# Performance work log

Hardware: AMD Instinct MI355X
Metric: run time of the kernel (lower is better)

## Reference

```python
import jax, jax.numpy as jnp
import numpy as np

B, S, H = 1, 2048, 2048
HD, NQ, NKV = 128, 16, 4
FFH = 8192
EPS = 1e-5
ROPE_BASE = 10000.0
SOFTMAX_CAP = 50.0
CLIP_L, CLIP_R = 0.0, 1.0


def setup_inputs() -> dict:
    key = jax.random.key(0)
    ks = jax.random.split(key, 10)
    std = 0.02
    return {
        "x": jax.random.normal(ks[0], (B, S, H), dtype=jnp.float32),
        "attn_norm_w": jax.random.uniform(ks[1], (H,), minval=-1.0, maxval=1.0, dtype=jnp.float32),
        "mlp_norm_w": jax.random.uniform(ks[2], (H,), minval=-1.0, maxval=1.0, dtype=jnp.float32),
        "wq": jax.random.normal(ks[3], (H, NQ * HD), dtype=jnp.float32) * std,
        "wk": jax.random.normal(ks[4], (H, NKV * HD), dtype=jnp.float32) * std,
        "wv": jax.random.normal(ks[5], (H, NKV * HD), dtype=jnp.float32) * std,
        "wo": jax.random.normal(ks[6], (NQ * HD, H), dtype=jnp.float32) * std,
        "w_gate": jax.random.normal(ks[7], (H, FFH), dtype=jnp.float32) * std,
        "w_up": jax.random.normal(ks[8], (H, FFH), dtype=jnp.float32) * std,
        "w_down": jax.random.normal(ks[9], (FFH, H), dtype=jnp.float32) * std,
    }


def _rms_norm(x, w):
    # GroupRMSNorm with group_size=None -> whole hidden dim
    var = jnp.mean(jnp.square(x), axis=-1, keepdims=True)
    return x * jax.lax.rsqrt(var + EPS) * w


def _rope_cos_sin(seq_len, dim):
    inv_freq = 1.0 / (ROPE_BASE ** (jnp.arange(0, dim, 2, dtype=jnp.float32) / dim))
    t = jnp.arange(seq_len, dtype=jnp.float32)
    freqs = jnp.outer(t, inv_freq)                      # [S, dim/2]
    emb = jnp.concatenate([freqs, freqs], axis=-1)      # [S, dim]
    return jnp.cos(emb), jnp.sin(emb)


def _apply_rope(x, cos, sin):
    # x: [B, S, h, d]; rotate-half (LLaMA-style)
    d = x.shape[-1]
    x1, x2 = x[..., : d // 2], x[..., d // 2 :]
    rot = jnp.concatenate([-x2, x1], axis=-1)
    return x * cos[None, :, None, :] + rot * sin[None, :, None, :]


def _qk_norm(x):
    # per-head RMS norm over head_dim (qk_norm_group_size == head_dim), unit weight
    var = jnp.mean(jnp.square(x), axis=-1, keepdims=True)
    return x * jax.lax.rsqrt(var + EPS)


def reference(x, attn_norm_w, mlp_norm_w, wq, wk, wv, wo, w_gate, w_up, w_down):
    # ---- attention sub-layer ----
    h = _rms_norm(x, attn_norm_w)                                     # [B,S,H]
    q = (h @ wq).reshape(B, S, NQ, HD)
    k = (h @ wk).reshape(B, S, NKV, HD)
    v = (h @ wv).reshape(B, S, NKV, HD)

    cos, sin = _rope_cos_sin(S, HD)
    q = _apply_rope(q, cos, sin)
    k = _apply_rope(k, cos, sin)

    q = _qk_norm(q)
    k = _qk_norm(k)

    # GQA: expand kv heads to match q heads
    rep = NQ // NKV
    k = jnp.repeat(k, rep, axis=2)                                    # [B,S,NQ,HD]
    v = jnp.repeat(v, rep, axis=2)

    scale = 1.0 / jnp.sqrt(jnp.float32(HD))
    scores = jnp.einsum("bshd,bthd->bhst", q, k) * scale              # [B,NQ,S,S]
    # softmax cap: cap * tanh(s / cap)
    scores = SOFTMAX_CAP * jnp.tanh(scores / SOFTMAX_CAP)
    causal = jnp.tril(jnp.ones((S, S), dtype=bool))
    scores = jnp.where(causal[None, None], scores, -jnp.inf)
    p = jax.nn.softmax(scores, axis=-1)
    # clip range (l, r): clamp(p * (r - l) + l, 0, 1)
    p = jnp.clip(p * (CLIP_R - CLIP_L) + CLIP_L, 0.0, 1.0)
    o = jnp.einsum("bhst,bthd->bshd", p, v).reshape(B, S, NQ * HD)
    x = x + o @ wo

    # ---- MLP sub-layer (gated SiLU) ----
    h2 = _rms_norm(x, mlp_norm_w)
    mlp_out = (jax.nn.silu(h2 @ w_gate) * (h2 @ w_up)) @ w_down
    return x + mlp_out
```

## Files before the change

kernel.cpp:

```cpp
#include <hip/hip_runtime.h>

typedef __bf16 bf16;
typedef __bf16 bf16x4 __attribute__((ext_vector_type(4)));
typedef __bf16 bf16x8 __attribute__((ext_vector_type(8)));
typedef float f32x4 __attribute__((ext_vector_type(4)));

#define GLP16(gp, lp) __builtin_amdgcn_global_load_lds( \
    (const __attribute__((address_space(1))) void*)(gp), \
    (__attribute__((address_space(3))) void*)(lp), 16, 0, 0)

__device__ __forceinline__ f32x4 mfma16(bf16x8 a, bf16x8 b, f32x4 c) {
    return __builtin_amdgcn_mfma_f32_16x16x32_bf16(a, b, c, 0, 0, 0);
}

__global__ __launch_bounds__(256) void k_rmsnorm(const float* __restrict__ x,
        const float* __restrict__ w, bf16* __restrict__ out) {
    const int H = 2048;
    size_t row = blockIdx.x;
    const float* xr = x + row * H;
    int base = threadIdx.x * 8;
    float4 a = *(const float4*)(xr + base);
    float4 b = *(const float4*)(xr + base + 4);
    float ss = a.x*a.x + a.y*a.y + a.z*a.z + a.w*a.w
             + b.x*b.x + b.y*b.y + b.z*b.z + b.w*b.w;
#pragma unroll
    for (int m = 32; m > 0; m >>= 1) ss += __shfl_xor(ss, m);
    __shared__ float red[4];
    if ((threadIdx.x & 63) == 0) red[threadIdx.x >> 6] = ss;
    __syncthreads();
    float tot = red[0] + red[1] + red[2] + red[3];
    float rs = rsqrtf(tot * (1.0f / H) + 1e-5f);
    float4 wa = *(const float4*)(w + base);
    float4 wb = *(const float4*)(w + base + 4);
    bf16x8 ov;
    ov[0] = (bf16)(a.x * rs * wa.x); ov[1] = (bf16)(a.y * rs * wa.y);
    ov[2] = (bf16)(a.z * rs * wa.z); ov[3] = (bf16)(a.w * rs * wa.w);
    ov[4] = (bf16)(b.x * rs * wb.x); ov[5] = (bf16)(b.y * rs * wb.y);
    ov[6] = (bf16)(b.z * rs * wb.z); ov[7] = (bf16)(b.w * rs * wb.w);
    *(bf16x8*)(out + row * H + base) = ov;
}

__global__ __launch_bounds__(256) void k_convT(const float* __restrict__ W,
        bf16* __restrict__ Wt, int K, int N, int rmul, int roff) {
    __shared__ float t[32][33];
    int k0 = blockIdx.x * 32, n0 = blockIdx.y * 32;
    int tx = threadIdx.x, ty = threadIdx.y;
#pragma unroll
    for (int i = 0; i < 4; i++)
        t[ty + i * 8][tx] = W[(size_t)(k0 + ty + i * 8) * N + n0 + tx];
    __syncthreads();
#pragma unroll
    for (int i = 0; i < 4; i++)
        Wt[((size_t)(n0 + ty + i * 8) * rmul + roff) * K + k0 + tx] =
            (bf16)t[tx][ty + i * 8];
}

__global__ __launch_bounds__(256) void k_transpose(const bf16* __restrict__ in,
        bf16* __restrict__ out, int R, int C) {
    __shared__ bf16 t[32][33];
    int r0 = blockIdx.x * 32, c0 = blockIdx.y * 32;
    int tx = threadIdx.x & 31, ty = threadIdx.x >> 5;
#pragma unroll
    for (int i = 0; i < 4; i++)
        t[ty + i * 8][tx] = in[(size_t)(r0 + ty + i * 8) * C + c0 + tx];
    __syncthreads();
#pragma unroll
    for (int i = 0; i < 4; i++)
        out[(size_t)(c0 + ty + i * 8) * R + r0 + tx] = t[tx][ty + i * 8];
}

template<int EPI>
__global__ __launch_bounds__(512, 2) void k_gemm5(const bf16* __restrict__ A,
        const bf16* __restrict__ Bt, void* __restrict__ outp,
        const void* __restrict__ aux, int M, int N, int K, int ksplit) {
    extern __shared__ char lds[];
    const int tid = threadIdx.x, wave = tid >> 6, lane = tid & 63;
    const int lr = lane & 15, kg = lane >> 4;
    const int wm = wave >> 2, wn = wave & 3;
    const int bn = blockIdx.x, bm = blockIdx.y, split = blockIdx.z;
    const int row0 = bm * 256, col0 = bn * 256;
    const int kbeg = split * ksplit;
    const int NT = ksplit >> 6;
    const size_t K2 = (size_t)K * 2;
    const int xorm = (lr & 7) << 4;

    char* const A0p = lds;
    char* const A1p = lds + 32768;
    char* const B0p = lds + 65536;
    char* const B1p = lds + 98304;

    size_t soff[2];
#pragma unroll
    for (int s = 0; s < 2; s++) {
        int d = s * 8192 + tid * 16;
        int rh = d >> 7, c = d & 127;
        soff[s] = (size_t)rh * K2 + (c ^ ((rh & 7) << 4));
    }
    const char* Ab = (const char*)A + ((size_t)row0 * K + kbeg) * 2;
    const char* Bb = (const char*)Bt + ((size_t)col0 * K + kbeg) * 2;

    auto stA = [&](int t, int mh) {
        const char* src = Ab + (size_t)(mh * 128) * K2 + (size_t)t * 128;
        char* dst = lds + (t & 1) * 32768 + mh * 16384 + wave * 1024;
        GLP16(src + soff[0], dst);
        GLP16(src + soff[1], dst + 8192);
    };
    auto stB = [&](int t, int nh) {
        const char* src = Bb + (size_t)(nh * 128) * K2 + (size_t)t * 128;
        char* dst = lds + 65536 + (t & 1) * 32768 + nh * 16384 + wave * 1024;
        GLP16(src + soff[0], dst);
        GLP16(src + soff[1], dst + 8192);
    };

    f32x4 acc[8][4];
#pragma unroll
    for (int m = 0; m < 8; m++)
#pragma unroll
        for (int n = 0; n < 4; n++) acc[m][n] = (f32x4){0, 0, 0, 0};

    bf16x8 a[8], c0[4], c1[4];
    auto rdA = [&](const char* base, int mh) {
#pragma unroll
        for (int mi = 0; mi < 4; mi++)
#pragma unroll
            for (int kk = 0; kk < 2; kk++) {
                int rh = wm * 64 + mi * 16 + lr;
                int c = (kk * 64 + kg * 16) ^ xorm;
                a[mi * 2 + kk] = *(const bf16x8*)(base + mh * 16384 + rh * 128 + c);
            }
    };
    auto rdB = [&](const char* base, int nh, bf16x8 (&b)[4]) {
#pragma unroll
        for (int nj = 0; nj < 2; nj++)
#pragma unroll
            for (int kk = 0; kk < 2; kk++) {
                int rh = wn * 32 + nj * 16 + lr;
                int c = (kk * 64 + kg * 16) ^ xorm;
                b[nj * 2 + kk] = *(const bf16x8*)(base + nh * 16384 + rh * 128 + c);
            }
    };
    auto mm = [&](int mh, int nh, bf16x8 (&b)[4]) {
#pragma unroll
        for (int mi = 0; mi < 4; mi++)
#pragma unroll
            for (int nj = 0; nj < 2; nj++)
#pragma unroll
                for (int kk = 0; kk < 2; kk++)
                    acc[mh * 4 + mi][nh * 2 + nj] =
                        mfma16(a[mi * 2 + kk], b[nj * 2 + kk],
                               acc[mh * 4 + mi][nh * 2 + nj]);
    };

#define PBAR do { asm volatile("" ::: "memory"); \
                  __builtin_amdgcn_s_barrier(); \
                  asm volatile("" ::: "memory"); } while (0)

    stA(0, 0); stB(0, 0); stB(0, 1); stA(0, 1);
    stA(1, 0); stB(1, 0); stB(1, 1);
    asm volatile("s_waitcnt vmcnt(6)" ::: "memory");
    PBAR;

    const int NIT = NT >> 1;
    for (int it = 0; it < NIT; ++it) {
        const int t = it * 2;
        const bool more = (t + 2 < NT);
        rdA(A0p, 0); rdB(B0p, 0, c0);
        stA(t + 1, 1);
        __builtin_amdgcn_s_setprio(1); mm(0, 0, c0); __builtin_amdgcn_s_setprio(0);
        PBAR;
        rdB(B0p, 1, c1);
        if (more) stA(t + 2, 0);
        __builtin_amdgcn_s_setprio(1); mm(0, 1, c1); __builtin_amdgcn_s_setprio(0);
        PBAR;
        rdA(A0p, 1);
        if (more) stB(t + 2, 0);
        __builtin_amdgcn_s_setprio(1); mm(1, 1, c1); __builtin_amdgcn_s_setprio(0);
        PBAR;
        if (more) stB(t + 2, 1);
        __builtin_amdgcn_s_setprio(1); mm(1, 0, c0); __builtin_amdgcn_s_setprio(0);
        if (more) asm volatile("s_waitcnt vmcnt(6)" ::: "memory");
        else      asm volatile("s_waitcnt vmcnt(0)" ::: "memory");
        PBAR;
        rdA(A1p, 0); rdB(B1p, 0, c0);
        if (more) stA(t + 2, 1);
        __builtin_amdgcn_s_setprio(1); mm(0, 0, c0); __builtin_amdgcn_s_setprio(0);
        PBAR;
        rdB(B1p, 1, c1);
        if (t + 3 < NT) stA(t + 3, 0);
        __builtin_amdgcn_s_setprio(1); mm(0, 1, c1); __builtin_amdgcn_s_setprio(0);
        PBAR;
        rdA(A1p, 1);
        if (t + 3 < NT) stB(t + 3, 0);
        __builtin_amdgcn_s_setprio(1); mm(1, 1, c1); __builtin_amdgcn_s_setprio(0);
        PBAR;
        if (t + 3 < NT) stB(t + 3, 1);
        __builtin_amdgcn_s_setprio(1); mm(1, 0, c0); __builtin_amdgcn_s_setprio(0);
        if (more) asm volatile("s_waitcnt vmcnt(6)" ::: "memory");
        PBAR;
    }
#undef PBAR

#pragma unroll
    for (int mi = 0; mi < 8; mi++)
#pragma unroll
        for (int ni = 0; ni < 4; ni++)
#pragma unroll
            for (int r = 0; r < 4; r++) {
                size_t row = row0 + (mi >> 2) * 128 + wm * 64 + (mi & 3) * 16 + kg * 4 + r;
                size_t col = col0 + (ni >> 1) * 128 + wn * 32 + (ni & 1) * 16 + lr;
                float vv = acc[mi][ni][r];
                if (EPI == 3) {
                    ((float*)outp)[(size_t)split * M * N + row * N + col] = vv;
                } else {
                    float pv = __shfl_xor(vv, 1);
                    float g = (lane & 1) ? pv : vv;
                    float u = (lane & 1) ? vv : pv;
                    float sg = g / (1.0f + __expf(-g));
                    if (!(lane & 1))
                        ((bf16*)outp)[row * (size_t)(N >> 1) + (col >> 1)] =
                            (bf16)(sg * u);
                }
            }
}

__global__ __launch_bounds__(256) void k_reduce(const float* __restrict__ parts,
        const float* __restrict__ resid, float* __restrict__ out,
        int ns, size_t n4) {
    size_t i = (size_t)blockIdx.x * 256 + threadIdx.x;
    if (i >= n4) return;
    float4 acc = ((const float4*)resid)[i];
    for (int s = 0; s < ns; s++) {
        float4 p = ((const float4*)(parts + (size_t)s * n4 * 4))[i];
        acc.x += p.x; acc.y += p.y; acc.z += p.z; acc.w += p.w;
    }
    ((float4*)out)[i] = acc;
}

__global__ __launch_bounds__(256) void k_reduce_rms(const float* __restrict__ parts,
        const float* __restrict__ resid, const float* __restrict__ w,
        float* __restrict__ x2, bf16* __restrict__ hb, int ns) {
    const int H = 2048;
    size_t row = blockIdx.x;
    int base = threadIdx.x * 8;
    const float* rr = resid + row * H + base;
    float4 a = *(const float4*)rr;
    float4 b = *(const float4*)(rr + 4);
    for (int s = 0; s < ns; s++) {
        const float* pp = parts + (size_t)s * H * 2048 + row * H + base;
        float4 pa = *(const float4*)pp;
        float4 pb = *(const float4*)(pp + 4);
        a.x += pa.x; a.y += pa.y; a.z += pa.z; a.w += pa.w;
        b.x += pb.x; b.y += pb.y; b.z += pb.z; b.w += pb.w;
    }
    *(float4*)(x2 + row * H + base) = a;
    *(float4*)(x2 + row * H + base + 4) = b;
    float ss = a.x*a.x + a.y*a.y + a.z*a.z + a.w*a.w
             + b.x*b.x + b.y*b.y + b.z*b.z + b.w*b.w;
#pragma unroll
    for (int m = 32; m > 0; m >>= 1) ss += __shfl_xor(ss, m);
    __shared__ float red[4];
    if ((threadIdx.x & 63) == 0) red[threadIdx.x >> 6] = ss;
    __syncthreads();
    float tot = red[0] + red[1] + red[2] + red[3];
    float rs = rsqrtf(tot * (1.0f / H) + 1e-5f);
    float4 wa = *(const float4*)(w + base);
    float4 wb = *(const float4*)(w + base + 4);
    bf16x8 ov;
    ov[0] = (bf16)(a.x * rs * wa.x); ov[1] = (bf16)(a.y * rs * wa.y);
    ov[2] = (bf16)(a.z * rs * wa.z); ov[3] = (bf16)(a.w * rs * wa.w);
    ov[4] = (bf16)(b.x * rs * wb.x); ov[5] = (bf16)(b.y * rs * wb.y);
    ov[6] = (bf16)(b.z * rs * wb.z); ov[7] = (bf16)(b.w * rs * wb.w);
    *(bf16x8*)(hb + row * H + base) = ov;
}

__global__ __launch_bounds__(256) void k_qkvfin(const float* __restrict__ parts,
        bf16* __restrict__ qb, bf16* __restrict__ kb, bf16* __restrict__ vb) {
    int s = blockIdx.x;
    int col = blockIdx.y * 1024 + threadIdx.x * 4;
    const float* p0 = parts + (size_t)s * 3072 + col;
    const float* p1 = p0 + (size_t)2048 * 3072;
    float4 a = *(const float4*)p0;
    float4 b = *(const float4*)p1;
    a.x += b.x; a.y += b.y; a.z += b.z; a.w += b.w;
    bf16x4 o;
    o[0] = (bf16)a.x; o[1] = (bf16)a.y; o[2] = (bf16)a.z; o[3] = (bf16)a.w;
    if (col < 2048)      *(bf16x4*)(qb + (size_t)s * 2048 + col) = o;
    else if (col < 2560) *(bf16x4*)(kb + (size_t)s * 512 + col - 2048) = o;
    else                 *(bf16x4*)(vb + (size_t)s * 512 + col - 2560) = o;
}

__global__ __launch_bounds__(256) void k_rope(bf16* __restrict__ q,
        bf16* __restrict__ k) {
    int s = blockIdx.x, lane = threadIdx.x & 63;
    int hid = blockIdx.y * 4 + (threadIdx.x >> 6);
    bf16* p;
    if (hid < 16) p = q + (size_t)s * 2048 + hid * 128;
    else          p = k + (size_t)s * 512 + (hid - 16) * 128;
    float x1 = (float)p[lane], x2 = (float)p[lane + 64];
    float f = exp2f((float)lane * -0.2076205059304601f);
    float sn, cs;
    sincosf((float)s * f, &sn, &cs);
    float o1 = x1 * cs - x2 * sn;
    float o2 = x2 * cs + x1 * sn;
    float ss = o1 * o1 + o2 * o2;
#pragma unroll
    for (int m = 32; m > 0; m >>= 1) ss += __shfl_xor(ss, m);
    float rs = rsqrtf(ss * (1.0f / 128.0f) + 1e-5f);
    p[lane] = (bf16)(o1 * rs);
    p[lane + 64] = (bf16)(o2 * rs);
}

__global__ __launch_bounds__(256) void k_attn(const bf16* __restrict__ qg,
        const bf16* __restrict__ kgl, const bf16* __restrict__ vtg,
        bf16* __restrict__ og) {
    extern __shared__ char alds[];
    int pi = blockIdx.x, h = blockIdx.y, kvh = h >> 2;
    int tid = threadIdx.x, wave = tid >> 6, lane = tid & 63;
    int lr = lane & 15, kgrp = lane >> 4;

    int rowQ[4], colQ[4], rowV[4], colV[4];
#pragma unroll
    for (int j = 0; j < 4; j++) {
        int p = j * 4096 + wave * 1024 + lane * 16;
        int ps = p ^ (((p >> 8) & 7) << 4);
        rowQ[j] = ps >> 8; colQ[j] = ps & 255;
        int pv = p ^ (((p >> 7) & 7) << 4);
        rowV[j] = pv >> 7; colV[j] = pv & 127;
    }

    const float C1 = 0.08838834764831845f / 50.0f;
    const float L2E50 = 72.13475204444817f;

#pragma unroll 1
    for (int half = 0; half < 2; ++half) {
        int qt = half ? (31 - pi) : pi;
        int nt = qt + 1;

#pragma unroll
        for (int j = 0; j < 4; j++)
            GLP16((const char*)qg + (size_t)(qt * 64 + rowQ[j]) * 4096 + h * 256 + colQ[j],
                  alds + j * 4096 + wave * 1024);
        for (int t = 0; t < 2 && t < nt; t++) {
#pragma unroll
            for (int j = 0; j < 4; j++)
                GLP16((const char*)kgl + (size_t)(t * 64 + rowQ[j]) * 1024 + kvh * 256 + colQ[j],
                      alds + 16384 + t * 16384 + j * 4096 + wave * 1024);
#pragma unroll
            for (int j = 0; j < 4; j++)
                GLP16((const char*)vtg + (size_t)(kvh * 128 + rowV[j]) * 4096 + t * 128 + colV[j],
                      alds + 49152 + t * 16384 + j * 4096 + wave * 1024);
        }
        if (nt > 1) asm volatile("s_waitcnt vmcnt(8)" ::: "memory");
        else        asm volatile("s_waitcnt vmcnt(0)" ::: "memory");
        __builtin_amdgcn_s_barrier();

        bf16x8 qf[4];
#pragma unroll
        for (int c = 0; c < 4; c++) {
            int b = (wave * 16 + lr) * 256 + c * 64 + kgrp * 16;
            qf[c] = *(const bf16x8*)(alds + (b ^ (((b >> 8) & 7) << 4)));
        }
        f32x4 accO[8];
#pragma unroll
        for (int n = 0; n < 8; n++) accO[n] = (f32x4){0, 0, 0, 0};
        float lsum[4] = {0, 0, 0, 0};
        int qrow = qt * 64 + wave * 16 + kgrp * 4;

        for (int kt = 0; kt < nt; kt++) {
            int buf = kt & 1;
            const char* Kb = alds + 16384 + buf * 16384;
            const char* Vb = alds + 49152 + buf * 16384;
            char* Pb = alds + 81920;
#pragma unroll
            for (int j = 0; j < 4; j++) {
                f32x4 s = {0, 0, 0, 0};
#pragma unroll
                for (int c = 0; c < 4; c++) {
                    int b = (j * 16 + lr) * 256 + c * 64 + kgrp * 16;
                    bf16x8 kf = *(const bf16x8*)(Kb + (b ^ (((b >> 8) & 7) << 4)));
                    s = mfma16(qf[c], kf, s);
                }
                int key = kt * 64 + j * 16 + lr;
#pragma unroll
                for (int r = 0; r < 4; r++) {
                    float y = s[r] * C1;
                    float y2 = y * y;
                    float u = fmaf(y2, 0.13333333f, -0.33333333f);
                    u = fmaf(y2, u, 1.0f);
                    float t5 = y * u;
                    float pe = fmaf(t5, L2E50, -L2E50);
                    float pv = (key <= qrow + r) ? exp2f(pe) : 0.0f;
                    lsum[r] += pv;
                    int wb = (wave * 16 + kgrp * 4 + r) * 128 + (j * 16 + lr) * 2;
                    *(bf16*)(Pb + (wb ^ (((wb >> 7) & 7) << 4))) = (bf16)pv;
                }
            }
            bf16x8 pf[2];
#pragma unroll
            for (int ks2 = 0; ks2 < 2; ks2++) {
                int b = (wave * 16 + lr) * 128 + ks2 * 64 + kgrp * 16;
                pf[ks2] = *(const bf16x8*)(Pb + (b ^ (((b >> 7) & 7) << 4)));
            }
#pragma unroll
            for (int n = 0; n < 8; n++)
#pragma unroll
                for (int ks2 = 0; ks2 < 2; ks2++) {
                    int b = (n * 16 + lr) * 128 + ks2 * 64 + kgrp * 16;
                    bf16x8 vf = *(const bf16x8*)(Vb + (b ^ (((b >> 7) & 7) << 4)));
                    accO[n] = mfma16(pf[ks2], vf, accO[n]);
                }
            __builtin_amdgcn_s_barrier();
            bool more = (kt + 2 < nt);
            if (more) {
                int t = kt + 2;
#pragma unroll
                for (int j = 0; j < 4; j++)
                    GLP16((const char*)kgl + (size_t)(t * 64 + rowQ[j]) * 1024 + kvh * 256 + colQ[j],
                          alds + 16384 + buf * 16384 + j * 4096 + wave * 1024);
#pragma unroll
                for (int j = 0; j < 4; j++)
                    GLP16((const char*)vtg + (size_t)(kvh * 128 + rowV[j]) * 4096 + t * 128 + colV[j],
                          alds + 49152 + buf * 16384 + j * 4096 + wave * 1024);
            }
            if (kt + 1 < nt) {
                if (more) asm volatile("s_waitcnt vmcnt(8)" ::: "memory");
                else      asm volatile("s_waitcnt vmcnt(0)" ::: "memory");
                __builtin_amdgcn_s_barrier();
            }
        }
#pragma unroll
        for (int r = 0; r < 4; r++) {
            float t = lsum[r];
            t += __shfl_xor(t, 1); t += __shfl_xor(t, 2);
            t += __shfl_xor(t, 4); t += __shfl_xor(t, 8);
            lsum[r] = t;
        }
#pragma unroll
        for (int n = 0; n < 8; n++)
#pragma unroll
            for (int r = 0; r < 4; r++) {
                size_t row = qt * 64 + wave * 16 + kgrp * 4 + r;
                og[row * 2048 + h * 128 + n * 16 + lr] = (bf16)(accO[n][r] / lsum[r]);
            }
    }
}

extern "C" void kernel_launch(void* const* d_in, const int* in_sizes, int n_in,
                              void* d_out, int out_size, void* d_ws, size_t ws_size,
                              hipStream_t stream) {
    const float* x      = (const float*)d_in[0];
    const float* attn_w = (const float*)d_in[1];
    const float* mlp_w  = (const float*)d_in[2];
    const float* wq     = (const float*)d_in[3];
    const float* wk     = (const float*)d_in[4];
    const float* wv     = (const float*)d_in[5];
    const float* wo     = (const float*)d_in[6];
    const float* wgate  = (const float*)d_in[7];
    const float* wup    = (const float*)d_in[8];
    const float* wdown  = (const float*)d_in[9];
    float* out = (float*)d_out;
    char* ws = (char*)d_ws;

    const size_t MB = 1024 * 1024;
    bf16* Wqkv = (bf16*)(ws + 0);
    bf16* vt   = (bf16*)(ws + 0);
    float* pO  = (float*)(ws + 0);
    bf16* Wgu  = (bf16*)(ws + 0);
    float* pD  = (float*)(ws + 0);
    bf16* WoT  = (bf16*)(ws + 64 * MB);
    bf16* WdT  = (bf16*)(ws + 64 * MB);
    bf16* hb   = (bf16*)(ws + 96 * MB);
    bf16* qb   = (bf16*)(ws + 104 * MB);
    bf16* kb   = (bf16*)(ws + 112 * MB);
    bf16* vb   = (bf16*)(ws + 114 * MB);
    bf16* ob   = (bf16*)(ws + 116 * MB);
    float* x2  = (float*)(ws + 124 * MB);
    bf16* gb   = (bf16*)(ws + 140 * MB);
    float* pQ  = (float*)(ws + 116 * MB);

    const int LDS5 = 131072;
    hipFuncSetAttribute((const void*)&k_gemm5<3>,
        hipFuncAttributeMaxDynamicSharedMemorySize, LDS5);
    hipFuncSetAttribute((const void*)&k_gemm5<4>,
        hipFuncAttributeMaxDynamicSharedMemorySize, LDS5);
    const int LDSA = 90112;
    hipFuncSetAttribute((const void*)&k_attn,
        hipFuncAttributeMaxDynamicSharedMemorySize, LDSA);

    dim3 cb(32, 8);
    const size_t n4 = (size_t)2048 * 2048 / 4;

    k_rmsnorm<<<2048, 256, 0, stream>>>(x, attn_w, hb);
    k_convT<<<dim3(64, 64), cb, 0, stream>>>(wq, Wqkv, 2048, 2048, 1, 0);
    k_convT<<<dim3(64, 16), cb, 0, stream>>>(wk, Wqkv + 4194304, 2048, 512, 1, 0);
    k_convT<<<dim3(64, 16), cb, 0, stream>>>(wv, Wqkv + 5242880, 2048, 512, 1, 0);
    k_gemm5<3><<<dim3(12, 8, 2), 512, LDS5, stream>>>(hb, Wqkv, pQ, nullptr,
                                                      2048, 3072, 2048, 1024);
    k_qkvfin<<<dim3(2048, 3), 256, 0, stream>>>(pQ, qb, kb, vb);
    k_transpose<<<dim3(64, 16), 256, 0, stream>>>(vb, vt, 2048, 512);
    k_rope<<<dim3(2048, 5), 256, 0, stream>>>(qb, kb);
    k_attn<<<dim3(16, 16), 256, LDSA, stream>>>(qb, kb, vt, ob);
    k_convT<<<dim3(64, 64), cb, 0, stream>>>(wo, WoT, 2048, 2048, 1, 0);
    k_gemm5<3><<<dim3(8, 8, 4), 512, LDS5, stream>>>(ob, WoT, pO, nullptr,
                                                     2048, 2048, 2048, 512);
    k_reduce_rms<<<2048, 256, 0, stream>>>(pO, x, mlp_w, x2, hb, 4);
    k_convT<<<dim3(64, 256), cb, 0, stream>>>(wgate, Wgu, 2048, 8192, 2, 0);
    k_convT<<<dim3(64, 256), cb, 0, stream>>>(wup, Wgu, 2048, 8192, 2, 1);
    k_gemm5<4><<<dim3(64, 8, 1), 512, LDS5, stream>>>(hb, Wgu, gb, nullptr,
                                                      2048, 16384, 2048, 2048);
    k_convT<<<dim3(256, 64), cb, 0, stream>>>(wdown, WdT, 8192, 2048, 1, 0);
    k_gemm5<3><<<dim3(8, 8, 4), 512, LDS5, stream>>>(gb, WdT, pD, nullptr,
                                                     2048, 2048, 8192, 2048);
    k_reduce<<<4096, 256, 0, stream>>>(pD, x2, out, 4, n4);
}
```

Baseline: 467.0 us.

## Restructure GEMM main loop into single-tile iterations with fewer barriers

Replaces the unrolled two-tile, eight-barrier-per-pair main loop of the bf16 MFMA GEMM with a one-tile-per-iteration loop that issues two MFMA quadrant groups per phase and uses only two barriers per K tile. Global-to-LDS prefetch is reordered so the next tile's halves load while the current tile computes, with adjusted vmcnt waits. It also handles odd tile counts. The aim is less barrier and synchronisation overhead and more MFMA work between waits. The risk is less latency hiding per phase or register pressure from holding more fragments live.

Result: slower. 484.2 us (+3.7%).

```diff
diff --git a/kernel.cpp b/kernel.cpp
--- a/kernel.cpp
+++ b/kernel.cpp
@@ -70,7 +70,7 @@
 }
 
 template<int EPI>
-__global__ __launch_bounds__(512, 2) void k_gemm5(const bf16* __restrict__ A,
+__global__ __launch_bounds__(512, 2) void k_gemm6(const bf16* __restrict__ A,
         const bf16* __restrict__ Bt, void* __restrict__ outp,
         const void* __restrict__ aux, int M, int N, int K, int ksplit) {
     extern __shared__ char lds[];
@@ -84,11 +84,6 @@
     const size_t K2 = (size_t)K * 2;
     const int xorm = (lr & 7) << 4;
 
-    char* const A0p = lds;
-    char* const A1p = lds + 32768;
-    char* const B0p = lds + 65536;
-    char* const B1p = lds + 98304;
-
     size_t soff[2];
 #pragma unroll
     for (int s = 0; s < 2; s++) {
@@ -156,46 +151,37 @@
                   asm volatile("" ::: "memory"); } while (0)
 
     stA(0, 0); stB(0, 0); stB(0, 1); stA(0, 1);
-    stA(1, 0); stB(1, 0); stB(1, 1);
-    asm volatile("s_waitcnt vmcnt(6)" ::: "memory");
+    if (NT > 1) {
+        stA(1, 0); stB(1, 0);
+        asm volatile("s_waitcnt vmcnt(4)" ::: "memory");
+    } else {
+        asm volatile("s_waitcnt vmcnt(0)" ::: "memory");
+    }
     PBAR;
-
-    const int NIT = NT >> 1;
-    for (int it = 0; it < NIT; ++it) {
-        const int t = it * 2;
-        const bool more = (t + 2 < NT);
-        rdA(A0p, 0); rdB(B0p, 0, c0);
-        stA(t + 1, 1);
-        __builtin_amdgcn_s_setprio(1); mm(0, 0, c0); __builtin_amdgcn_s_setprio(0);
+    rdA(lds, 0);
+    rdB(lds + 65536, 0, c0);
+
+    for (int t = 0; t < NT; ++t) {
+        const char* Acur = lds + (t & 1) * 32768;
+        const char* Bcur = lds + 65536 + (t & 1) * 32768;
+        const char* Anxt = lds + ((t + 1) & 1) * 32768;
+        const char* Bnxt = lds + 65536 + ((t + 1) & 1) * 32768;
+        const bool m1 = (t + 1 < NT), m2 = (t + 2 < NT);
+        rdB(Bcur, 1, c1);
+        if (m1) { stB(t + 1, 1); stA(t + 1, 1); }
+        __builtin_amdgcn_s_setprio(1);
+        mm(0, 0, c0); mm(0, 1, c1);
+        __builtin_amdgcn_s_setprio(0);
+        rdA(Acur, 1);
+        if (m1) asm volatile("s_waitcnt vmcnt(2)" ::: "memory");
         PBAR;
-        rdB(B0p, 1, c1);
-        if (more) stA(t + 2, 0);
-        __builtin_amdgcn_s_setprio(1); mm(0, 1, c1); __builtin_amdgcn_s_setprio(0);
-        PBAR;
-        rdA(A0p, 1);
-        if (more) stB(t + 2, 0);
-        __builtin_amdgcn_s_setprio(1); mm(1, 1, c1); __builtin_amdgcn_s_setprio(0);
-        PBAR;
-        if (more) stB(t + 2, 1);
-        __builtin_amdgcn_s_setprio(1); mm(1, 0, c0); __builtin_amdgcn_s_setprio(0);
-        if (more) asm volatile("s_waitcnt vmcnt(6)" ::: "memory");
-        else      asm volatile("s_waitcnt vmcnt(0)" ::: "memory");
-        PBAR;
-        rdA(A1p, 0); rdB(B1p, 0, c0);
-        if (more) stA(t + 2, 1);
-        __builtin_amdgcn_s_setprio(1); mm(0, 0, c0); __builtin_amdgcn_s_setprio(0);
-        PBAR;
-        rdB(B1p, 1, c1);
-        if (t + 3 < NT) stA(t + 3, 0);
-        __builtin_amdgcn_s_setprio(1); mm(0, 1, c1); __builtin_amdgcn_s_setprio(0);
-        PBAR;
-        rdA(A1p, 1);
-        if (t + 3 < NT) stB(t + 3, 0);
-        __builtin_amdgcn_s_setprio(1); mm(1, 1, c1); __builtin_amdgcn_s_setprio(0);
-        PBAR;
-        if (t + 3 < NT) stB(t + 3, 1);
-        __builtin_amdgcn_s_setprio(1); mm(1, 0, c0); __builtin_amdgcn_s_setprio(0);
-        if (more) asm volatile("s_waitcnt vmcnt(6)" ::: "memory");
+        __builtin_amdgcn_s_setprio(1);
+        mm(1, 1, c1); mm(1, 0, c0);
+        __builtin_amdgcn_s_setprio(0);
+        if (m1) { rdA(Anxt, 0); rdB(Bnxt, 0, c0); }
+        if (m2) { stA(t + 2, 0); stB(t + 2, 0); }
+        if (m2)      asm volatile("s_waitcnt vmcnt(2)" ::: "memory");
+        else if (m1) asm volatile("s_waitcnt vmcnt(0)" ::: "memory");
         PBAR;
     }
 #undef PBAR
@@ -478,11 +464,11 @@
     bf16* gb   = (bf16*)(ws + 140 * MB);
     float* pQ  = (float*)(ws + 116 * MB);
 
-    const int LDS5 = 131072;
-    hipFuncSetAttribute((const void*)&k_gemm5<3>,
-        hipFuncAttributeMaxDynamicSharedMemorySize, LDS5);
-    hipFuncSetAttribute((const void*)&k_gemm5<4>,
-        hipFuncAttributeMaxDynamicSharedMemorySize, LDS5);
+    const int LDS6 = 131072;
+    hipFuncSetAttribute((const void*)&k_gemm6<3>,
+        hipFuncAttributeMaxDynamicSharedMemorySize, LDS6);
+    hipFuncSetAttribute((const void*)&k_gemm6<4>,
+        hipFuncAttributeMaxDynamicSharedMemorySize, LDS6);
     const int LDSA = 90112;
     hipFuncSetAttribute((const void*)&k_attn,
         hipFuncAttributeMaxDynamicSharedMemorySize, LDSA);
@@ -494,22 +480,22 @@
     k_convT<<<dim3(64, 64), cb, 0, stream>>>(wq, Wqkv, 2048, 2048, 1, 0);
     k_convT<<<dim3(64, 16), cb, 0, stream>>>(wk, Wqkv + 4194304, 2048, 512, 1, 0);
     k_convT<<<dim3(64, 16), cb, 0, stream>>>(wv, Wqkv + 5242880, 2048, 512, 1, 0);
-    k_gemm5<3><<<dim3(12, 8, 2), 512, LDS5, stream>>>(hb, Wqkv, pQ, nullptr,
+    k_gemm6<3><<<dim3(12, 8, 2), 512, LDS6, stream>>>(hb, Wqkv, pQ, nullptr,
                                                       2048, 3072, 2048, 1024);
     k_qkvfin<<<dim3(2048, 3), 256, 0, stream>>>(pQ, qb, kb, vb);
     k_transpose<<<dim3(64, 16), 256, 0, stream>>>(vb, vt, 2048, 512);
     k_rope<<<dim3(2048, 5), 256, 0, stream>>>(qb, kb);
     k_attn<<<dim3(16, 16), 256, LDSA, stream>>>(qb, kb, vt, ob);
     k_convT<<<dim3(64, 64), cb, 0, stream>>>(wo, WoT, 2048, 2048, 1, 0);
-    k_gemm5<3><<<dim3(8, 8, 4), 512, LDS5, stream>>>(ob, WoT, pO, nullptr,
+    k_gemm6<3><<<dim3(8, 8, 4), 512, LDS6, stream>>>(ob, WoT, pO, nullptr,
                                                      2048, 2048, 2048, 512);
     k_reduce_rms<<<2048, 256, 0, stream>>>(pO, x, mlp_w, x2, hb, 4);
     k_convT<<<dim3(64, 256), cb, 0, stream>>>(wgate, Wgu, 2048, 8192, 2, 0);
     k_convT<<<dim3(64, 256), cb, 0, stream>>>(wup, Wgu, 2048, 8192, 2, 1);
-    k_gemm5<4><<<dim3(64, 8, 1), 512, LDS5, stream>>>(hb, Wgu, gb, nullptr,
+    k_gemm6<4><<<dim3(64, 8, 1), 512, LDS6, stream>>>(hb, Wgu, gb, nullptr,
                                                       2048, 16384, 2048, 2048);
     k_convT<<<dim3(256, 64), cb, 0, stream>>>(wdown, WdT, 8192, 2048, 1, 0);
-    k_gemm5<3><<<dim3(8, 8, 4), 512, LDS5, stream>>>(gb, WdT, pD, nullptr,
+    k_gemm6<3><<<dim3(8, 8, 4), 512, LDS6, stream>>>(gb, WdT, pD, nullptr,
                                                      2048, 2048, 8192, 2048);
     k_reduce<<<4096, 256, 0, stream>>>(pD, x2, out, 4, n4);
 }
```
